# Kernel tuning notes

Hardware: AMD Instinct MI355X
Metric: run time of the kernel (lower is better)

Reference implementation:

```python
import jax, jax.numpy as jnp
import numpy as np

N = 131072      # points (rays x samples chunk)
E = 8           # spatial sub-networks (centroids)
DIN = 90        # encoded pos+dir features fed to sub-NeRFs (xyz_real=True -> x[:, 3:])
H = 256         # sub-NeRF hidden width
DOUT = 4        # rgb + sigma
MARGIN = 2.0    # boundary_margin
EPS = 1e-8


def setup_inputs() -> dict:
    key = jax.random.key(0)
    k = jax.random.split(key, 5)
    x_xyz = jax.random.uniform(k[0], (N, 3), dtype=jnp.float32)          # routing coords in [0,1)^3
    x_feat = jax.random.normal(k[1], (N, DIN), dtype=jnp.float32)        # encoded features
    x = jnp.concatenate([x_xyz, x_feat], axis=1)                         # [N, 3+DIN]
    centroids = jax.random.uniform(k[2], (E, 3), dtype=jnp.float32)
    W1 = jax.random.normal(k[3], (E, DIN, H), dtype=jnp.float32) * 0.05
    b1 = jnp.zeros((E, H), dtype=jnp.float32)
    W2 = jax.random.normal(k[4], (E, H, DOUT), dtype=jnp.float32) * 0.05
    b2 = jnp.zeros((E, DOUT), dtype=jnp.float32)
    return {"x": x, "centroids": centroids, "W1": W1, "b1": b1, "W2": W2, "b2": b2}


def reference(x, centroids, W1, b1, W2, b2):
    # --- centroid routing (torch.cdist equivalent) ---
    xyz = x[:, :3]                                                       # [N,3]
    d2 = jnp.sum((xyz[:, None, :] - centroids[None, :, :]) ** 2, axis=-1)
    dist = jnp.sqrt(jnp.maximum(d2, 0.0))                                # [N,E]
    inv = 1.0 / (dist + EPS)
    min_d = jnp.min(dist, axis=1, keepdims=True)                         # [N,1]
    inv = jnp.where(dist > MARGIN * min_d, 0.0, inv)                     # zero far experts
    weights = inv / jnp.sum(inv, axis=-1, keepdims=True)                 # [N,E], rows sum to 1

    # --- per-expert sub-NeRF MLP, weighted combine ---
    # Dense-equivalent of masked gather + weighted scatter-add: experts whose
    # weight is exactly 0 contribute nothing, matching the torch masked path.
    feat = x[:, 3:]                                                      # xyz_real=True -> drop xyz
    h = jax.nn.relu(jnp.einsum('nd,edh->enh', feat, W1) + b1[:, None, :])  # [E,N,H]
    out_e = jnp.einsum('enh,eho->eno', h, W2) + b2[:, None, :]             # [E,N,DOUT]
    return jnp.einsum('eno,ne->no', out_e, weights)                        # [N,DOUT]
```

## Files before the change

### kernel.cpp

```cpp
#include <hip/hip_runtime.h>

#define NPTS 131072
#define NE 8
#define DIN 90
#define NH 256
#define NGMAX 2304

typedef __attribute__((ext_vector_type(8))) short bf16x8;
typedef __attribute__((ext_vector_type(4))) float f32x4;
typedef __attribute__((ext_vector_type(2))) float f32x2;
typedef __attribute__((ext_vector_type(4))) unsigned int u32x4;
typedef __attribute__((ext_vector_type(2))) unsigned int u32x2;
typedef __attribute__((ext_vector_type(4), aligned(4))) float f32x4a;
typedef __attribute__((ext_vector_type(2), aligned(4))) float f32x2a;

#define WS_W1T   0
#define WS_W2T   393216
#define WS_PERM  458752
#define WS_BKTB  983040
#define WS_HIST  984064
#define WS_CUR   985088
#define WS_GTB   986112
#define WS_GTM   995328
#define WS_END   1004544

__device__ __forceinline__ unsigned short f2bf(float f) {
  unsigned int u = __float_as_uint(f);
  u += 0x7fffu + ((u >> 16) & 1u);
  return (unsigned short)(u >> 16);
}

#if defined(__has_builtin) && __has_builtin(__builtin_amdgcn_cvt_pk_bf16_f32)
typedef __attribute__((ext_vector_type(2))) __bf16 bf16x2;
__device__ __forceinline__ unsigned int pkbf(float f0, float f1) {
  bf16x2 r = __builtin_amdgcn_cvt_pk_bf16_f32(f0, f1);
  return __builtin_bit_cast(unsigned int, r);
}
#else
__device__ __forceinline__ unsigned int pkbf(float f0, float f1) {
  unsigned int u0 = __float_as_uint(f0) + 0x7fffu;
  unsigned int u1 = __float_as_uint(f1) + 0x7fffu;
  return __builtin_amdgcn_perm(u1, u0, 0x07060302u);
}
#endif

__device__ __forceinline__ bf16x8 cvt8(f32x4 a, f32x4 b) {
  u32x4 r;
  r[0] = pkbf(a[0], a[1]);
  r[1] = pkbf(a[2], a[3]);
  r[2] = pkbf(b[0], b[1]);
  r[3] = pkbf(b[2], b[3]);
  return __builtin_bit_cast(bf16x8, r);
}

__device__ __forceinline__ int pmask(const float* __restrict__ gx,
                                     const float* __restrict__ cent) {
  float px = gx[0], py = gx[1], pz = gx[2];
  float d[NE];
  float mind = 3.4e38f;
#pragma unroll
  for (int e = 0; e < NE; ++e) {
    float dx = px - cent[e * 3 + 0];
    float dy = py - cent[e * 3 + 1];
    float dz = pz - cent[e * 3 + 2];
    float d2 = dx * dx + dy * dy + dz * dz;
    d[e] = sqrtf(fmaxf(d2, 0.f));
    mind = fminf(mind, d[e]);
  }
  int m = 0;
#pragma unroll
  for (int e = 0; e < NE; ++e)
    if (!(d[e] > 2.0f * mind)) m |= (1 << e);
  return m;
}

__global__ __launch_bounds__(512) void zerok(int* __restrict__ p) {
  p[threadIdx.x] = 0;
}

__global__ __launch_bounds__(256) void prep_mask(
    const float* __restrict__ W1, const float* __restrict__ W2,
    const float* __restrict__ x, const float* __restrict__ cent,
    unsigned short* __restrict__ W1T, unsigned short* __restrict__ W2T,
    int* __restrict__ hist) {
  const int t = threadIdx.x;
  const int blk = blockIdx.x;
  __shared__ unsigned int shm[64 * 49];
  if (blk < 32) {
    const int e = blk >> 2;
    const int n0 = (blk & 3) * 64;
    const int nl = t & 63;
    const int kq = t >> 6;
#pragma unroll
    for (int j = 0; j < 12; ++j) {
      const int kp2 = kq + 4 * j;
      const int k0 = 2 * kp2, k1 = k0 + 1;
      unsigned int lo = 0, hi = 0;
      if (k0 < DIN) lo = f2bf(W1[((size_t)e * DIN + k0) * NH + n0 + nl]);
      if (k1 < DIN) hi = f2bf(W1[((size_t)e * DIN + k1) * NH + n0 + nl]);
      shm[nl * 49 + kp2] = lo | (hi << 16);
    }
    __syncthreads();
    unsigned int* dst = (unsigned int*)(W1T + (size_t)(e * NH + n0) * 96);
#pragma unroll
    for (int j = 0; j < 12; ++j) {
      const int u = t + 256 * j;
      dst[u] = shm[(u / 48) * 49 + (u % 48)];
    }
  } else if (blk < 40) {
    const int e = blk - 32;
    unsigned int* dst = (unsigned int*)W2T + (size_t)e * 2048;
    const float* src = W2 + (size_t)e * 1024;
#pragma unroll
    for (int j = 0; j < 8; ++j) {
      const int u = t + 256 * j;
      const int o = u >> 7, kp = u & 127;
      unsigned int v = 0;
      if (o < 4) {
        unsigned int lo = f2bf(src[(2 * kp) * 4 + o]);
        unsigned int hi = f2bf(src[(2 * kp + 1) * 4 + o]);
        v = lo | (hi << 16);
      }
      dst[u] = v;
    }
  } else {
    int* lh = (int*)shm;
    lh[t] = 0;
    __syncthreads();
    const int base = (blk - 40) * 1024;
#pragma unroll
    for (int j = 0; j < 4; ++j) {
      const int m = pmask(x + (size_t)(base + j * 256 + t) * 93, cent);
      atomicAdd(&lh[m], 1);
    }
    __syncthreads();
    if (lh[t] > 0) atomicAdd(&hist[t], lh[t]);
  }
}

__global__ __launch_bounds__(256) void scank(const int* __restrict__ hist,
                                             int* __restrict__ bktb,
                                             int* __restrict__ gt_base,
                                             int* __restrict__ gt_meta) {
  __shared__ int s1[256], s2[256];
  const int t = threadIdx.x;
  const int c = hist[t];
  s1[t] = c;
  __syncthreads();
  for (int off = 1; off < 256; off <<= 1) {
    int a = s1[t];
    int b = (t >= off) ? s1[t - off] : 0;
    __syncthreads();
    s1[t] = a + b;
    __syncthreads();
  }
  const int base = s1[t] - c;
  bktb[t] = base;
  const int gc = (c + 63) >> 6;
  s2[t] = gc;
  __syncthreads();
  for (int off = 1; off < 256; off <<= 1) {
    int a = s2[t];
    int b = (t >= off) ? s2[t - off] : 0;
    __syncthreads();
    s2[t] = a + b;
    __syncthreads();
  }
  const int goff = s2[t] - gc;
  for (int j = 0; j < gc; ++j) {
    const int rem = c - 64 * j;
    gt_base[goff + j] = base + 64 * j;
    gt_meta[goff + j] = t | ((rem < 64 ? rem : 64) << 8);
  }
  __syncthreads();
  const int total = s2[255];
  for (int s = total + t; s < NGMAX; s += 256) gt_meta[s] = 0;
}

__global__ __launch_bounds__(256) void scatterk(const float* __restrict__ x,
                                                const float* __restrict__ cent,
                                                const int* __restrict__ bktb,
                                                int* __restrict__ cursor,
                                                int* __restrict__ perm) {
  __shared__ int lh[256], lb[256], lc[256];
  const int t = threadIdx.x;
  lh[t] = 0;
  lc[t] = 0;
  __syncthreads();
  const int base = blockIdx.x * 1024;
  int m[4];
#pragma unroll
  for (int j = 0; j < 4; ++j) {
    m[j] = pmask(x + (size_t)(base + j * 256 + t) * 93, cent);
    atomicAdd(&lh[m[j]], 1);
  }
  __syncthreads();
  if (lh[t] > 0) lb[t] = bktb[t] + atomicAdd(&cursor[t], lh[t]);
  __syncthreads();
#pragma unroll
  for (int j = 0; j < 4; ++j) {
    const int p = base + j * 256 + t;
    const int lp = atomicAdd(&lc[m[j]], 1);
    perm[lb[m[j]] + lp] = p;
  }
}

#define UNRL _Pragma("unroll")

#define LOADW1(E_, C_, D0, D1, D2, D3, D4, D5)                                  \
  do {                                                                          \
    const unsigned short* _p =                                                  \
        W1T + (size_t)((E_) * NH + 128 * (C_) + 32 * wid + l15) * 96 + 8 * l4;  \
    D0 = *(const bf16x8*)(_p);                                                  \
    D1 = *(const bf16x8*)(_p + 32);                                             \
    D2 = *(const bf16x8*)(_p + 64);                                             \
    D3 = *(const bf16x8*)(_p + 1536);                                           \
    D4 = *(const bf16x8*)(_p + 1568);                                           \
    D5 = *(const bf16x8*)(_p + 1600);                                           \
  } while (0)

#define LOADBW(E_, C_, D)                                                       \
  do {                                                                          \
    D = *(const bf16x8*)(W2T + (size_t)((E_) * 16 + l15) * NH + 128 * (C_) +    \
                         32 * wid + 8 * l4);                                    \
  } while (0)

#define EPI(MF)                                                                 \
  UNRL for (int nf = 0; nf < 4; ++nf) {                                         \
    const float _w = wv[nf];                                                    \
    f32x4 _a = acc[nf];                                                         \
    f32x2 _p0, _p1;                                                             \
    _p0[0] = _a[0]; _p0[1] = _a[1];                                             \
    _p1[0] = _a[2]; _p1[1] = _a[3];                                             \
    const f32x2 _z = {0.f, 0.f};                                                \
    _p0 = __builtin_elementwise_max(_p0, _z) * _w;                              \
    _p1 = __builtin_elementwise_max(_p1, _z) * _w;                              \
    u32x2 _pk;                                                                  \
    _pk[0] = pkbf(_p0[0], _p0[1]);                                              \
    _pk[1] = pkbf(_p1[0], _p1[1]);                                              \
    *(u32x2*)&sH[gbase + (nf * 64 + (l15 + 16 * (2 * (MF) + (l4 >> 1)))) * 8 +  \
                 4 * (l4 & 1)] = _pk;                                           \
  }

#define STEP(E_, C_, LDWV_, EP_, CP_, CW0, CW1, CW2, CW3, CW4, CW5, CBW,        \
             NW0, NW1, NW2, NW3, NW4, NW5, NBW)                                 \
  do {                                                                          \
    const int _cb = 128 * (C_) + 32 * wid;                                      \
    f32x4 _b1v0 = *(const f32x4*)&sB1[(E_) * NH + _cb + 4 * l4];                \
    f32x4 _b1v1 = *(const f32x4*)&sB1[(E_) * NH + _cb + 16 + 4 * l4];           \
    if (LDWV_) {                                                                \
      UNRL for (int nf = 0; nf < 4; ++nf) wv[nf] = sW[(E_)][16 * nf + l15];     \
    }                                                                           \
    LOADBW(EP_, CP_, NBW);                                                      \
    LOADW1(EP_, CP_, NW0, NW1, NW2, NW3, NW4, NW5);                             \
    {                                                                           \
      f32x4 acc[4];                                                             \
      __builtin_amdgcn_s_setprio(1);                                            \
      UNRL for (int nf = 0; nf < 4; ++nf)                                       \
          acc[nf] = __builtin_amdgcn_mfma_f32_16x16x32_bf16(CW0, bfr[nf][0],    \
                                                            _b1v0, 0, 0, 0);    \
      UNRL for (int nf = 0; nf < 4; ++nf)                                       \
          acc[nf] = __builtin_amdgcn_mfma_f32_16x16x32_bf16(CW1, bfr[nf][1],    \
                                                            acc[nf], 0, 0, 0);  \
      UNRL for (int nf = 0; nf < 4; ++nf)                                       \
          acc[nf] = __builtin_amdgcn_mfma_f32_16x16x32_bf16(CW2, bfr[nf][2],    \
                                                            acc[nf], 0, 0, 0);  \
      __builtin_amdgcn_s_setprio(0);                                            \
      EPI(0)                                                                    \
      __builtin_amdgcn_s_setprio(1);                                            \
      UNRL for (int nf = 0; nf < 4; ++nf)                                       \
          acc[nf] = __builtin_amdgcn_mfma_f32_16x16x32_bf16(CW3, bfr[nf][0],    \
                                                            _b1v1, 0, 0, 0);    \
      UNRL for (int nf = 0; nf < 4; ++nf)                                       \
          acc[nf] = __builtin_amdgcn_mfma_f32_16x16x32_bf16(CW4, bfr[nf][1],    \
                                                            acc[nf], 0, 0, 0);  \
      UNRL for (int nf = 0; nf < 4; ++nf)                                       \
          acc[nf] = __builtin_amdgcn_mfma_f32_16x16x32_bf16(CW5, bfr[nf][2],    \
                                                            acc[nf], 0, 0, 0);  \
      __builtin_amdgcn_s_setprio(0);                                            \
      EPI(1)                                                                    \
    }                                                                           \
    __builtin_amdgcn_s_setprio(1);                                              \
    UNRL for (int rf = 0; rf < 4; ++rf) {                                       \
      bf16x8 _ah = *(const bf16x8*)&sH[gbase + (rf * 64 + lane) * 8];           \
      facc[rf] = __builtin_amdgcn_mfma_f32_16x16x32_bf16(_ah, CBW, facc[rf],    \
                                                         0, 0, 0);              \
    }                                                                           \
    __builtin_amdgcn_s_setprio(0);                                              \
  } while (0)

__global__ __launch_bounds__(256, 3) void main_sparse(
    const float* __restrict__ x, const float* __restrict__ cent,
    const float* __restrict__ b1, const float* __restrict__ b2,
    const unsigned short* __restrict__ W1T, const unsigned short* __restrict__ W2T,
    const int* __restrict__ perm, const int* __restrict__ gt_base,
    const int* __restrict__ gt_meta, float* __restrict__ out) {
  const int meta = gt_meta[blockIdx.x];
  const int cnt = meta >> 8;
  if (cnt == 0) return;
  const int gmask = meta & 255;
  const int base = gt_base[blockIdx.x];

  __shared__ unsigned short sH[4 * 2048];
  __shared__ float sW[NE][64];
  __shared__ float sB2[64][4];
  __shared__ float sB1[NE * NH];
  __shared__ int sIdx[64];
  __shared__ int sElist[9];

  const int t    = threadIdx.x;
  const int lane = t & 63;
  const int wid  = t >> 6;
  const int l15  = lane & 15;
  const int l4   = lane >> 4;
  const int gbase = wid * 2048;

#pragma unroll
  for (int j = 0; j < 2; ++j)
    *(f32x4*)&sB1[t * 4 + j * 1024] = *(const f32x4a*)&b1[t * 4 + j * 1024];
  if (t < 64) sIdx[t] = perm[base + (t < cnt ? t : cnt - 1)];
  if (t == 0) {
    int ne = 0;
#pragma unroll
    for (int e = 0; e < NE; ++e)
      if ((gmask >> e) & 1) sElist[ne++] = e;
    sElist[8] = ne;
  }
  __syncthreads();

  bf16x8 bfr[4][3];
#pragma unroll
  for (int nf = 0; nf < 4; ++nf) {
    const float* gr = x + (size_t)sIdx[16 * nf + l15] * 93 + 3;
    f32x4 v0, v1;
    v0 = *(const f32x4a*)(gr + 8 * l4);
    v1 = *(const f32x4a*)(gr + 8 * l4 + 4);
    bfr[nf][0] = cvt8(v0, v1);
    v0 = *(const f32x4a*)(gr + 32 + 8 * l4);
    v1 = *(const f32x4a*)(gr + 36 + 8 * l4);
    bfr[nf][1] = cvt8(v0, v1);
    if (l4 < 3) {
      v0 = *(const f32x4a*)(gr + 64 + 8 * l4);
      v1 = *(const f32x4a*)(gr + 68 + 8 * l4);
    } else {
      f32x2 tl = *(const f32x2a*)(gr + 88);
      v0[0] = tl[0]; v0[1] = tl[1]; v0[2] = 0.f; v0[3] = 0.f;
      v1[0] = 0.f; v1[1] = 0.f; v1[2] = 0.f; v1[3] = 0.f;
    }
    bfr[nf][2] = cvt8(v0, v1);
  }

  if (t < 64) {
    const float* gx = x + (size_t)sIdx[t] * 93;
    float px = gx[0], py = gx[1], pz = gx[2];
    float dist[NE], inv[NE];
    float mind = 3.4e38f;
#pragma unroll
    for (int e = 0; e < NE; ++e) {
      float dx = px - cent[e * 3 + 0];
      float dy = py - cent[e * 3 + 1];
      float dz = pz - cent[e * 3 + 2];
      float d2 = dx * dx + dy * dy + dz * dz;
      float d = sqrtf(fmaxf(d2, 0.f));
      dist[e] = d;
      inv[e] = 1.f / (d + 1e-8f);
      mind = fminf(mind, d);
    }
    float s = 0.f;
#pragma unroll
    for (int e = 0; e < NE; ++e) {
      if (dist[e] > 2.0f * mind) inv[e] = 0.f;
      s += inv[e];
    }
    float rs = 1.f / s;
    float bb[4] = {0.f, 0.f, 0.f, 0.f};
#pragma unroll
    for (int e = 0; e < NE; ++e) {
      float w = inv[e] * rs;
      sW[e][t] = w;
#pragma unroll
      for (int o = 0; o < 4; ++o) bb[o] += w * b2[e * 4 + o];
    }
#pragma unroll
    for (int o = 0; o < 4; ++o) sB2[t][o] = bb[o];
  }
  __syncthreads();

  const int niter = 2 * sElist[8];

  bf16x8 w1A0, w1A1, w1A2, w1A3, w1A4, w1A5;
  bf16x8 w1B0, w1B1, w1B2, w1B3, w1B4, w1B5;
  bf16x8 bwA, bwB;
  float wv[4];
  f32x4 facc[4] = {{0.f, 0.f, 0.f, 0.f}, {0.f, 0.f, 0.f, 0.f},
                   {0.f, 0.f, 0.f, 0.f}, {0.f, 0.f, 0.f, 0.f}};

  {
    const int e0 = sElist[0];
    LOADBW(e0, 0, bwA);
    LOADW1(e0, 0, w1A0, w1A1, w1A2, w1A3, w1A4, w1A5);
  }

  for (int i = 0; i < niter; i += 2) {
    const int e = sElist[i >> 1];
    const int ip2 = (i + 2 < niter) ? (i + 2) : (i + 1);
    const int e2 = sElist[ip2 >> 1];
    const int c2 = ip2 & 1;
    STEP(e, 0, 1, e, 1, w1A0, w1A1, w1A2, w1A3, w1A4, w1A5, bwA,
         w1B0, w1B1, w1B2, w1B3, w1B4, w1B5, bwB);
    STEP(e, 1, 0, e2, c2, w1B0, w1B1, w1B2, w1B3, w1B4, w1B5, bwB,
         w1A0, w1A1, w1A2, w1A3, w1A4, w1A5, bwA);
  }

  __syncthreads();
  float* sOutP = (float*)sH;
  if (l15 < 4) {
#pragma unroll
    for (int rf = 0; rf < 4; ++rf)
#pragma unroll
      for (int r = 0; r < 4; ++r)
        sOutP[(wid * 64 + 16 * rf + 4 * l4 + r) * 4 + l15] = facc[rf][r];
  }
  __syncthreads();
  {
    const int row = t >> 2, o = t & 3;
    if (row < cnt) {
      float v = sB2[row][o] + sOutP[(0 * 64 + row) * 4 + o] +
                sOutP[(1 * 64 + row) * 4 + o] + sOutP[(2 * 64 + row) * 4 + o] +
                sOutP[(3 * 64 + row) * 4 + o];
      out[(size_t)sIdx[row] * 4 + o] = v;
    }
  }
}

__global__ __launch_bounds__(256, 3) void meganerf_main(
    const float* __restrict__ x, const float* __restrict__ cent,
    const float* __restrict__ b1, const float* __restrict__ b2,
    const unsigned short* __restrict__ W1T, const unsigned short* __restrict__ W2T,
    float* __restrict__ out) {
  __shared__ unsigned short sH[4 * 2048];
  __shared__ float sW[NE][64];
  __shared__ float sB2[64][4];
  __shared__ float sB1[NE * NH];

  const int t    = threadIdx.x;
  const int lane = t & 63;
  const int wid  = t >> 6;
  const int l15  = lane & 15;
  const int l4   = lane >> 4;
  const int row0 = blockIdx.x * 64;
  const int gbase = wid * 2048;

#pragma unroll
  for (int j = 0; j < 2; ++j)
    *(f32x4*)&sB1[t * 4 + j * 1024] = *(const f32x4a*)&b1[t * 4 + j * 1024];

  bf16x8 bfr[4][3];
#pragma unroll
  for (int nf = 0; nf < 4; ++nf) {
    const float* gr = x + (size_t)(row0 + 16 * nf + l15) * 93 + 3;
    f32x4 v0, v1;
    v0 = *(const f32x4a*)(gr + 8 * l4);
    v1 = *(const f32x4a*)(gr + 8 * l4 + 4);
    bfr[nf][0] = cvt8(v0, v1);
    v0 = *(const f32x4a*)(gr + 32 + 8 * l4);
    v1 = *(const f32x4a*)(gr + 36 + 8 * l4);
    bfr[nf][1] = cvt8(v0, v1);
    if (l4 < 3) {
      v0 = *(const f32x4a*)(gr + 64 + 8 * l4);
      v1 = *(const f32x4a*)(gr + 68 + 8 * l4);
    } else {
      f32x2 tl = *(const f32x2a*)(gr + 88);
      v0[0] = tl[0]; v0[1] = tl[1]; v0[2] = 0.f; v0[3] = 0.f;
      v1[0] = 0.f; v1[1] = 0.f; v1[2] = 0.f; v1[3] = 0.f;
    }
    bfr[nf][2] = cvt8(v0, v1);
  }

  if (t < 64) {
    const float* gx = x + (size_t)(row0 + t) * 93;
    float px = gx[0], py = gx[1], pz = gx[2];
    float dist[NE], inv[NE];
    float mind = 3.4e38f;
#pragma unroll
    for (int e = 0; e < NE; ++e) {
      float dx = px - cent[e * 3 + 0];
      float dy = py - cent[e * 3 + 1];
      float dz = pz - cent[e * 3 + 2];
      float d2 = dx * dx + dy * dy + dz * dz;
      float d = sqrtf(fmaxf(d2, 0.f));
      dist[e] = d;
      inv[e] = 1.f / (d + 1e-8f);
      mind = fminf(mind, d);
    }
    float s = 0.f;
#pragma unroll
    for (int e = 0; e < NE; ++e) {
      if (dist[e] > 2.0f * mind) inv[e] = 0.f;
      s += inv[e];
    }
    float rs = 1.f / s;
    float bb[4] = {0.f, 0.f, 0.f, 0.f};
#pragma unroll
    for (int e = 0; e < NE; ++e) {
      float w = inv[e] * rs;
      sW[e][t] = w;
#pragma unroll
      for (int o = 0; o < 4; ++o) bb[o] += w * b2[e * 4 + o];
    }
#pragma unroll
    for (int o = 0; o < 4; ++o) sB2[t][o] = bb[o];
  }
  __syncthreads();

  bf16x8 w1A0, w1A1, w1A2, w1A3, w1A4, w1A5;
  bf16x8 w1B0, w1B1, w1B2, w1B3, w1B4, w1B5;
  bf16x8 bwA, bwB;
  float wv[4];
  f32x4 facc[4] = {{0.f, 0.f, 0.f, 0.f}, {0.f, 0.f, 0.f, 0.f},
                   {0.f, 0.f, 0.f, 0.f}, {0.f, 0.f, 0.f, 0.f}};

  LOADBW(0, 0, bwA);
  LOADW1(0, 0, w1A0, w1A1, w1A2, w1A3, w1A4, w1A5);

  for (int i = 0; i < 16; i += 2) {
    const int e = i >> 1;
    const int ip2 = (i + 2) & 15;
    const int e2 = ip2 >> 1;
    STEP(e, 0, 1, e, 1, w1A0, w1A1, w1A2, w1A3, w1A4, w1A5, bwA,
         w1B0, w1B1, w1B2, w1B3, w1B4, w1B5, bwB);
    STEP(e, 1, 0, e2, 0, w1B0, w1B1, w1B2, w1B3, w1B4, w1B5, bwB,
         w1A0, w1A1, w1A2, w1A3, w1A4, w1A5, bwA);
  }

  __syncthreads();
  float* sOutP = (float*)sH;
  if (l15 < 4) {
#pragma unroll
    for (int rf = 0; rf < 4; ++rf)
#pragma unroll
      for (int r = 0; r < 4; ++r)
        sOutP[(wid * 64 + 16 * rf + 4 * l4 + r) * 4 + l15] = facc[rf][r];
  }
  __syncthreads();
  {
    const int row = t >> 2, o = t & 3;
    float v = sB2[row][o] + sOutP[(0 * 64 + row) * 4 + o] + sOutP[(1 * 64 + row) * 4 + o] +
              sOutP[(2 * 64 + row) * 4 + o] + sOutP[(3 * 64 + row) * 4 + o];
    out[row0 * 4 + t] = v;
  }
}

extern "C" void kernel_launch(void* const* d_in, const int* in_sizes, int n_in,
                              void* d_out, int out_size, void* d_ws, size_t ws_size,
                              hipStream_t stream) {
  const float* x    = (const float*)d_in[0];
  const float* cent = (const float*)d_in[1];
  const float* W1   = (const float*)d_in[2];
  const float* b1   = (const float*)d_in[3];
  const float* W2   = (const float*)d_in[4];
  const float* b2   = (const float*)d_in[5];
  float* out = (float*)d_out;

  char* ws = (char*)d_ws;
  unsigned short* W1T = (unsigned short*)(ws + WS_W1T);
  unsigned short* W2T = (unsigned short*)(ws + WS_W2T);
  int* perm   = (int*)(ws + WS_PERM);
  int* bktb   = (int*)(ws + WS_BKTB);
  int* hist   = (int*)(ws + WS_HIST);
  int* cursor = (int*)(ws + WS_CUR);
  int* gtb    = (int*)(ws + WS_GTB);
  int* gtm    = (int*)(ws + WS_GTM);

  if (ws_size >= (size_t)WS_END) {
    zerok<<<1, 512, 0, stream>>>(hist);
    prep_mask<<<168, 256, 0, stream>>>(W1, W2, x, cent, W1T, W2T, hist);
    scank<<<1, 256, 0, stream>>>(hist, bktb, gtb, gtm);
    scatterk<<<128, 256, 0, stream>>>(x, cent, bktb, cursor, perm);
    main_sparse<<<NGMAX, 256, 0, stream>>>(x, cent, b1, b2, W1T, W2T, perm, gtb,
                                           gtm, out);
  } else {
    prep_mask<<<40, 256, 0, stream>>>(W1, W2, x, cent, W1T, W2T, hist);
    meganerf_main<<<NPTS / 64, 256, 0, stream>>>(x, cent, b1, b2, W1T, W2T, out);
  }
}
```

Measured before the change: 173.3 us.

## Fuse routing pipeline into one cooperative persistent kernel with grid syncs

```diff
diff --git a/kernel.cpp b/kernel.cpp
--- a/kernel.cpp
+++ b/kernel.cpp
@@ -1,10 +1,13 @@
 #include <hip/hip_runtime.h>
+#include <hip/hip_cooperative_groups.h>
 
 #define NPTS 131072
 #define NE 8
 #define DIN 90
 #define NH 256
 #define NGMAX 2304
+
+namespace cg = cooperative_groups;
 
 typedef __attribute__((ext_vector_type(8))) short bf16x8;
 typedef __attribute__((ext_vector_type(4))) float f32x4;
@@ -17,12 +20,12 @@
 #define WS_W1T   0
 #define WS_W2T   393216
 #define WS_PERM  458752
-#define WS_BKTB  983040
-#define WS_HIST  984064
-#define WS_CUR   985088
-#define WS_GTB   986112
-#define WS_GTM   995328
-#define WS_END   1004544
+#define WS_PHIST 983040
+#define WS_BKTB  1114112
+#define WS_CUR   1115136
+#define WS_GTB   1116160
+#define WS_GTM   1125376
+#define WS_END   1134592
 
 __device__ __forceinline__ unsigned short f2bf(float f) {
   unsigned int u = __float_as_uint(f);
@@ -72,137 +75,6 @@
   for (int e = 0; e < NE; ++e)
     if (!(d[e] > 2.0f * mind)) m |= (1 << e);
   return m;
-}
-
-__global__ __launch_bounds__(512) void zerok(int* __restrict__ p) {
-  p[threadIdx.x] = 0;
-}
-
-__global__ __launch_bounds__(256) void prep_mask(
-    const float* __restrict__ W1, const float* __restrict__ W2,
-    const float* __restrict__ x, const float* __restrict__ cent,
-    unsigned short* __restrict__ W1T, unsigned short* __restrict__ W2T,
-    int* __restrict__ hist) {
-  const int t = threadIdx.x;
-  const int blk = blockIdx.x;
-  __shared__ unsigned int shm[64 * 49];
-  if (blk < 32) {
-    const int e = blk >> 2;
-    const int n0 = (blk & 3) * 64;
-    const int nl = t & 63;
-    const int kq = t >> 6;
-#pragma unroll
-    for (int j = 0; j < 12; ++j) {
-      const int kp2 = kq + 4 * j;
-      const int k0 = 2 * kp2, k1 = k0 + 1;
-      unsigned int lo = 0, hi = 0;
-      if (k0 < DIN) lo = f2bf(W1[((size_t)e * DIN + k0) * NH + n0 + nl]);
-      if (k1 < DIN) hi = f2bf(W1[((size_t)e * DIN + k1) * NH + n0 + nl]);
-      shm[nl * 49 + kp2] = lo | (hi << 16);
-    }
-    __syncthreads();
-    unsigned int* dst = (unsigned int*)(W1T + (size_t)(e * NH + n0) * 96);
-#pragma unroll
-    for (int j = 0; j < 12; ++j) {
-      const int u = t + 256 * j;
-      dst[u] = shm[(u / 48) * 49 + (u % 48)];
-    }
-  } else if (blk < 40) {
-    const int e = blk - 32;
-    unsigned int* dst = (unsigned int*)W2T + (size_t)e * 2048;
-    const float* src = W2 + (size_t)e * 1024;
-#pragma unroll
-    for (int j = 0; j < 8; ++j) {
-      const int u = t + 256 * j;
-      const int o = u >> 7, kp = u & 127;
-      unsigned int v = 0;
-      if (o < 4) {
-        unsigned int lo = f2bf(src[(2 * kp) * 4 + o]);
-        unsigned int hi = f2bf(src[(2 * kp + 1) * 4 + o]);
-        v = lo | (hi << 16);
-      }
-      dst[u] = v;
-    }
-  } else {
-    int* lh = (int*)shm;
-    lh[t] = 0;
-    __syncthreads();
-    const int base = (blk - 40) * 1024;
-#pragma unroll
-    for (int j = 0; j < 4; ++j) {
-      const int m = pmask(x + (size_t)(base + j * 256 + t) * 93, cent);
-      atomicAdd(&lh[m], 1);
-    }
-    __syncthreads();
-    if (lh[t] > 0) atomicAdd(&hist[t], lh[t]);
-  }
-}
-
-__global__ __launch_bounds__(256) void scank(const int* __restrict__ hist,
-                                             int* __restrict__ bktb,
-                                             int* __restrict__ gt_base,
-                                             int* __restrict__ gt_meta) {
-  __shared__ int s1[256], s2[256];
-  const int t = threadIdx.x;
-  const int c = hist[t];
-  s1[t] = c;
-  __syncthreads();
-  for (int off = 1; off < 256; off <<= 1) {
-    int a = s1[t];
-    int b = (t >= off) ? s1[t - off] : 0;
-    __syncthreads();
-    s1[t] = a + b;
-    __syncthreads();
-  }
-  const int base = s1[t] - c;
-  bktb[t] = base;
-  const int gc = (c + 63) >> 6;
-  s2[t] = gc;
-  __syncthreads();
-  for (int off = 1; off < 256; off <<= 1) {
-    int a = s2[t];
-    int b = (t >= off) ? s2[t - off] : 0;
-    __syncthreads();
-    s2[t] = a + b;
-    __syncthreads();
-  }
-  const int goff = s2[t] - gc;
-  for (int j = 0; j < gc; ++j) {
-    const int rem = c - 64 * j;
-    gt_base[goff + j] = base + 64 * j;
-    gt_meta[goff + j] = t | ((rem < 64 ? rem : 64) << 8);
-  }
-  __syncthreads();
-  const int total = s2[255];
-  for (int s = total + t; s < NGMAX; s += 256) gt_meta[s] = 0;
-}
-
-__global__ __launch_bounds__(256) void scatterk(const float* __restrict__ x,
-                                                const float* __restrict__ cent,
-                                                const int* __restrict__ bktb,
-                                                int* __restrict__ cursor,
-                                                int* __restrict__ perm) {
-  __shared__ int lh[256], lb[256], lc[256];
-  const int t = threadIdx.x;
-  lh[t] = 0;
-  lc[t] = 0;
-  __syncthreads();
-  const int base = blockIdx.x * 1024;
-  int m[4];
-#pragma unroll
-  for (int j = 0; j < 4; ++j) {
-    m[j] = pmask(x + (size_t)(base + j * 256 + t) * 93, cent);
-    atomicAdd(&lh[m[j]], 1);
-  }
-  __syncthreads();
-  if (lh[t] > 0) lb[t] = bktb[t] + atomicAdd(&cursor[t], lh[t]);
-  __syncthreads();
-#pragma unroll
-  for (int j = 0; j < 4; ++j) {
-    const int p = base + j * 256 + t;
-    const int lp = atomicAdd(&lc[m[j]], 1);
-    perm[lb[m[j]] + lp] = p;
-  }
 }
 
 #define UNRL _Pragma("unroll")
@@ -289,17 +161,18 @@
     __builtin_amdgcn_s_setprio(0);                                              \
   } while (0)
 
-__global__ __launch_bounds__(256, 3) void main_sparse(
+__global__ __launch_bounds__(256, 3) void mega2(
     const float* __restrict__ x, const float* __restrict__ cent,
     const float* __restrict__ b1, const float* __restrict__ b2,
-    const unsigned short* __restrict__ W1T, const unsigned short* __restrict__ W2T,
-    const int* __restrict__ perm, const int* __restrict__ gt_base,
-    const int* __restrict__ gt_meta, float* __restrict__ out) {
-  const int meta = gt_meta[blockIdx.x];
-  const int cnt = meta >> 8;
-  if (cnt == 0) return;
-  const int gmask = meta & 255;
-  const int base = gt_base[blockIdx.x];
+    const float* __restrict__ W1, const float* __restrict__ W2,
+    float* __restrict__ out,
+    unsigned short* __restrict__ W1T, unsigned short* __restrict__ W2T,
+    int* __restrict__ perm, int* __restrict__ phist, int* __restrict__ bktb,
+    int* __restrict__ cursor, int* __restrict__ gt_base,
+    int* __restrict__ gt_meta) {
+  cg::grid_group gg = cg::this_grid();
+  const int t   = threadIdx.x;
+  const int blk = blockIdx.x;
 
   __shared__ unsigned short sH[4 * 2048];
   __shared__ float sW[NE][64];
@@ -308,7 +181,124 @@
   __shared__ int sIdx[64];
   __shared__ int sElist[9];
 
-  const int t    = threadIdx.x;
+  if (blk < 32) {
+    const int e = blk >> 2;
+    const int n0 = (blk & 3) * 64;
+    unsigned int* ld = (unsigned int*)sH;
+    const int nl = t & 63;
+    const int kq = t >> 6;
+#pragma unroll
+    for (int j = 0; j < 12; ++j) {
+      const int kp2 = kq + 4 * j;
+      const int k0 = 2 * kp2, k1 = k0 + 1;
+      unsigned int lo = 0, hi = 0;
+      if (k0 < DIN) lo = f2bf(W1[((size_t)e * DIN + k0) * NH + n0 + nl]);
+      if (k1 < DIN) hi = f2bf(W1[((size_t)e * DIN + k1) * NH + n0 + nl]);
+      ld[nl * 49 + kp2] = lo | (hi << 16);
+    }
+    __syncthreads();
+    unsigned int* dst = (unsigned int*)(W1T + (size_t)(e * NH + n0) * 96);
+#pragma unroll
+    for (int j = 0; j < 12; ++j) {
+      const int u = t + 256 * j;
+      dst[u] = ld[(u / 48) * 49 + (u % 48)];
+    }
+  } else if (blk < 40) {
+    const int e = blk - 32;
+    unsigned int* dst = (unsigned int*)W2T + (size_t)e * 2048;
+    const float* src = W2 + (size_t)e * 1024;
+#pragma unroll
+    for (int j = 0; j < 8; ++j) {
+      const int u = t + 256 * j;
+      const int o = u >> 7, kp = u & 127;
+      unsigned int v = 0;
+      if (o < 4) {
+        unsigned int lo = f2bf(src[(2 * kp) * 4 + o]);
+        unsigned int hi = f2bf(src[(2 * kp + 1) * 4 + o]);
+        v = lo | (hi << 16);
+      }
+      dst[u] = v;
+    }
+  } else if (blk < 168) {
+    int* lh = (int*)sH;
+    lh[t] = 0;
+    __syncthreads();
+    const int base = (blk - 40) * 1024;
+#pragma unroll
+    for (int j = 0; j < 4; ++j) {
+      const int m = pmask(x + (size_t)(base + j * 256 + t) * 93, cent);
+      atomicAdd(&lh[m], 1);
+    }
+    __syncthreads();
+    phist[(blk - 40) * 256 + t] = lh[t];
+  }
+  gg.sync();
+
+  if (blk == 0) {
+    int* s1 = (int*)sH;
+    int* s2 = (int*)sH + 256;
+    int c = 0;
+    for (int b = 0; b < 128; ++b) c += phist[b * 256 + t];
+    s1[t] = c;
+    __syncthreads();
+    for (int off = 1; off < 256; off <<= 1) {
+      int a = s1[t];
+      int bb = (t >= off) ? s1[t - off] : 0;
+      __syncthreads();
+      s1[t] = a + bb;
+      __syncthreads();
+    }
+    const int base = s1[t] - c;
+    bktb[t] = base;
+    const int gc = (c + 63) >> 6;
+    s2[t] = gc;
+    __syncthreads();
+    for (int off = 1; off < 256; off <<= 1) {
+      int a = s2[t];
+      int bb = (t >= off) ? s2[t - off] : 0;
+      __syncthreads();
+      s2[t] = a + bb;
+      __syncthreads();
+    }
+    const int goff = s2[t] - gc;
+    for (int j = 0; j < gc; ++j) {
+      const int rem = c - 64 * j;
+      gt_base[goff + j] = base + 64 * j;
+      gt_meta[goff + j] = t | ((rem < 64 ? rem : 64) << 8);
+    }
+    cursor[t] = 0;
+    __syncthreads();
+    const int total = s2[255];
+    for (int s = total + t; s < NGMAX; s += 256) gt_meta[s] = 0;
+  }
+  gg.sync();
+
+  if (blk < 128) {
+    int* lh = (int*)sH;
+    int* lb = (int*)sH + 256;
+    int* lc = (int*)sH + 512;
+    lh[t] = 0;
+    lc[t] = 0;
+    __syncthreads();
+    const int base = blk * 1024;
+    int m[4];
+#pragma unroll
+    for (int j = 0; j < 4; ++j) {
+      m[j] = pmask(x + (size_t)(base + j * 256 + t) * 93, cent);
+      atomicAdd(&lh[m[j]], 1);
+    }
+    __syncthreads();
+    if (lh[t] > 0) lb[t] = bktb[t] + atomicAdd(&cursor[t], lh[t]);
+    __syncthreads();
+#pragma unroll
+    for (int j = 0; j < 4; ++j) {
+      const int p = base + j * 256 + t;
+      const int lp = atomicAdd(&lc[m[j]], 1);
+      perm[lb[m[j]] + lp] = p;
+    }
+  }
+  gg.sync();
+
   const int lane = t & 63;
   const int wid  = t >> 6;
   const int l15  = lane & 15;
@@ -318,117 +308,174 @@
 #pragma unroll
   for (int j = 0; j < 2; ++j)
     *(f32x4*)&sB1[t * 4 + j * 1024] = *(const f32x4a*)&b1[t * 4 + j * 1024];
-  if (t < 64) sIdx[t] = perm[base + (t < cnt ? t : cnt - 1)];
-  if (t == 0) {
-    int ne = 0;
-#pragma unroll
-    for (int e = 0; e < NE; ++e)
-      if ((gmask >> e) & 1) sElist[ne++] = e;
-    sElist[8] = ne;
-  }
-  __syncthreads();
-
-  bf16x8 bfr[4][3];
-#pragma unroll
-  for (int nf = 0; nf < 4; ++nf) {
-    const float* gr = x + (size_t)sIdx[16 * nf + l15] * 93 + 3;
-    f32x4 v0, v1;
-    v0 = *(const f32x4a*)(gr + 8 * l4);
-    v1 = *(const f32x4a*)(gr + 8 * l4 + 4);
-    bfr[nf][0] = cvt8(v0, v1);
-    v0 = *(const f32x4a*)(gr + 32 + 8 * l4);
-    v1 = *(const f32x4a*)(gr + 36 + 8 * l4);
-    bfr[nf][1] = cvt8(v0, v1);
-    if (l4 < 3) {
-      v0 = *(const f32x4a*)(gr + 64 + 8 * l4);
-      v1 = *(const f32x4a*)(gr + 68 + 8 * l4);
-    } else {
-      f32x2 tl = *(const f32x2a*)(gr + 88);
-      v0[0] = tl[0]; v0[1] = tl[1]; v0[2] = 0.f; v0[3] = 0.f;
-      v1[0] = 0.f; v1[1] = 0.f; v1[2] = 0.f; v1[3] = 0.f;
-    }
-    bfr[nf][2] = cvt8(v0, v1);
-  }
-
-  if (t < 64) {
-    const float* gx = x + (size_t)sIdx[t] * 93;
-    float px = gx[0], py = gx[1], pz = gx[2];
-    float dist[NE], inv[NE];
-    float mind = 3.4e38f;
-#pragma unroll
-    for (int e = 0; e < NE; ++e) {
-      float dx = px - cent[e * 3 + 0];
-      float dy = py - cent[e * 3 + 1];
-      float dz = pz - cent[e * 3 + 2];
-      float d2 = dx * dx + dy * dy + dz * dz;
-      float d = sqrtf(fmaxf(d2, 0.f));
-      dist[e] = d;
-      inv[e] = 1.f / (d + 1e-8f);
-      mind = fminf(mind, d);
-    }
-    float s = 0.f;
-#pragma unroll
-    for (int e = 0; e < NE; ++e) {
-      if (dist[e] > 2.0f * mind) inv[e] = 0.f;
-      s += inv[e];
-    }
-    float rs = 1.f / s;
-    float bb[4] = {0.f, 0.f, 0.f, 0.f};
-#pragma unroll
-    for (int e = 0; e < NE; ++e) {
-      float w = inv[e] * rs;
-      sW[e][t] = w;
-#pragma unroll
-      for (int o = 0; o < 4; ++o) bb[o] += w * b2[e * 4 + o];
-    }
-#pragma unroll
-    for (int o = 0; o < 4; ++o) sB2[t][o] = bb[o];
-  }
-  __syncthreads();
-
-  const int niter = 2 * sElist[8];
-
-  bf16x8 w1A0, w1A1, w1A2, w1A3, w1A4, w1A5;
-  bf16x8 w1B0, w1B1, w1B2, w1B3, w1B4, w1B5;
-  bf16x8 bwA, bwB;
-  float wv[4];
-  f32x4 facc[4] = {{0.f, 0.f, 0.f, 0.f}, {0.f, 0.f, 0.f, 0.f},
-                   {0.f, 0.f, 0.f, 0.f}, {0.f, 0.f, 0.f, 0.f}};
-
-  {
-    const int e0 = sElist[0];
-    LOADBW(e0, 0, bwA);
-    LOADW1(e0, 0, w1A0, w1A1, w1A2, w1A3, w1A4, w1A5);
-  }
-
-  for (int i = 0; i < niter; i += 2) {
-    const int e = sElist[i >> 1];
-    const int ip2 = (i + 2 < niter) ? (i + 2) : (i + 1);
-    const int e2 = sElist[ip2 >> 1];
-    const int c2 = ip2 & 1;
-    STEP(e, 0, 1, e, 1, w1A0, w1A1, w1A2, w1A3, w1A4, w1A5, bwA,
-         w1B0, w1B1, w1B2, w1B3, w1B4, w1B5, bwB);
-    STEP(e, 1, 0, e2, c2, w1B0, w1B1, w1B2, w1B3, w1B4, w1B5, bwB,
-         w1A0, w1A1, w1A2, w1A3, w1A4, w1A5, bwA);
-  }
-
-  __syncthreads();
-  float* sOutP = (float*)sH;
-  if (l15 < 4) {
-#pragma unroll
-    for (int rf = 0; rf < 4; ++rf)
-#pragma unroll
-      for (int r = 0; r < 4; ++r)
-        sOutP[(wid * 64 + 16 * rf + 4 * l4 + r) * 4 + l15] = facc[rf][r];
-  }
-  __syncthreads();
-  {
-    const int row = t >> 2, o = t & 3;
-    if (row < cnt) {
-      float v = sB2[row][o] + sOutP[(0 * 64 + row) * 4 + o] +
-                sOutP[(1 * 64 + row) * 4 + o] + sOutP[(2 * 64 + row) * 4 + o] +
-                sOutP[(3 * 64 + row) * 4 + o];
-      out[(size_t)sIdx[row] * 4 + o] = v;
+
+  for (int g = blk; g < NGMAX; g += gridDim.x) {
+    const int meta = gt_meta[g];
+    const int cnt = meta >> 8;
+    if (cnt == 0) continue;
+    const int gmask = meta & 255;
+    const int base = gt_base[g];
+
+    __syncthreads();
+    if (t < 64) sIdx[t] = perm[base + (t < cnt ? t : cnt - 1)];
+    if (t == 0) {
+      int ne = 0;
+#pragma unroll
+      for (int e = 0; e < NE; ++e)
+        if ((gmask >> e) & 1) sElist[ne++] = e;
+      sElist[8] = ne;
+    }
+    __syncthreads();
+
+    bf16x8 bfr[4][3];
+#pragma unroll
+    for (int nf = 0; nf < 4; ++nf) {
+      const float* gr = x + (size_t)sIdx[16 * nf + l15] * 93 + 3;
+      f32x4 v0, v1;
+      v0 = *(const f32x4a*)(gr + 8 * l4);
+      v1 = *(const f32x4a*)(gr + 8 * l4 + 4);
+      bfr[nf][0] = cvt8(v0, v1);
+      v0 = *(const f32x4a*)(gr + 32 + 8 * l4);
+      v1 = *(const f32x4a*)(gr + 36 + 8 * l4);
+      bfr[nf][1] = cvt8(v0, v1);
+      if (l4 < 3) {
+        v0 = *(const f32x4a*)(gr + 64 + 8 * l4);
+        v1 = *(const f32x4a*)(gr + 68 + 8 * l4);
+      } else {
+        f32x2 tl = *(const f32x2a*)(gr + 88);
+        v0[0] = tl[0]; v0[1] = tl[1]; v0[2] = 0.f; v0[3] = 0.f;
+        v1[0] = 0.f; v1[1] = 0.f; v1[2] = 0.f; v1[3] = 0.f;
+      }
+      bfr[nf][2] = cvt8(v0, v1);
+    }
+
+    if (t < 64) {
+      const float* gx = x + (size_t)sIdx[t] * 93;
+      float px = gx[0], py = gx[1], pz = gx[2];
+      float dist[NE], inv[NE];
+      float mind = 3.4e38f;
+#pragma unroll
+      for (int e = 0; e < NE; ++e) {
+        float dx = px - cent[e * 3 + 0];
+        float dy = py - cent[e * 3 + 1];
+        float dz = pz - cent[e * 3 + 2];
+        float d2 = dx * dx + dy * dy + dz * dz;
+        float d = sqrtf(fmaxf(d2, 0.f));
+        dist[e] = d;
+        inv[e] = 1.f / (d + 1e-8f);
+        mind = fminf(mind, d);
+      }
+      float s = 0.f;
+#pragma unroll
+      for (int e = 0; e < NE; ++e) {
+        if (dist[e] > 2.0f * mind) inv[e] = 0.f;
+        s += inv[e];
+      }
+      float rs = 1.f / s;
+      float bb[4] = {0.f, 0.f, 0.f, 0.f};
+#pragma unroll
+      for (int e = 0; e < NE; ++e) {
+        float w = inv[e] * rs;
+        sW[e][t] = w;
+#pragma unroll
+        for (int o = 0; o < 4; ++o) bb[o] += w * b2[e * 4 + o];
+      }
+#pragma unroll
+      for (int o = 0; o < 4; ++o) sB2[t][o] = bb[o];
+    }
+    __syncthreads();
+
+    const int niter = 2 * sElist[8];
+
+    bf16x8 w1A0, w1A1, w1A2, w1A3, w1A4, w1A5;
+    bf16x8 w1B0, w1B1, w1B2, w1B3, w1B4, w1B5;
+    bf16x8 bwA, bwB;
+    float wv[4];
+    f32x4 facc[4] = {{0.f, 0.f, 0.f, 0.f}, {0.f, 0.f, 0.f, 0.f},
+                     {0.f, 0.f, 0.f, 0.f}, {0.f, 0.f, 0.f, 0.f}};
+
+    {
+      const int e0 = sElist[0];
+      LOADBW(e0, 0, bwA);
+      LOADW1(e0, 0, w1A0, w1A1, w1A2, w1A3, w1A4, w1A5);
+    }
+
+    for (int i = 0; i < niter; i += 2) {
+      const int e = sElist[i >> 1];
+      const int ip2 = (i + 2 < niter) ? (i + 2) : (i + 1);
+      const int e2 = sElist[ip2 >> 1];
+      const int c2 = ip2 & 1;
+      STEP(e, 0, 1, e, 1, w1A0, w1A1, w1A2, w1A3, w1A4, w1A5, bwA,
+           w1B0, w1B1, w1B2, w1B3, w1B4, w1B5, bwB);
+      STEP(e, 1, 0, e2, c2, w1B0, w1B1, w1B2, w1B3, w1B4, w1B5, bwB,
+           w1A0, w1A1, w1A2, w1A3, w1A4, w1A5, bwA);
+    }
+
+    __syncthreads();
+    float* sOutP = (float*)sH;
+    if (l15 < 4) {
+#pragma unroll
+      for (int rf = 0; rf < 4; ++rf)
+#pragma unroll
+        for (int r = 0; r < 4; ++r)
+          sOutP[(wid * 64 + 16 * rf + 4 * l4 + r) * 4 + l15] = facc[rf][r];
+    }
+    __syncthreads();
+    {
+      const int row = t >> 2, o = t & 3;
+      if (row < cnt) {
+        float v = sB2[row][o] + sOutP[(0 * 64 + row) * 4 + o] +
+                  sOutP[(1 * 64 + row) * 4 + o] + sOutP[(2 * 64 + row) * 4 + o] +
+                  sOutP[(3 * 64 + row) * 4 + o];
+        out[(size_t)sIdx[row] * 4 + o] = v;
+      }
+    }
+  }
+}
+
+__global__ __launch_bounds__(256) void prep(const float* __restrict__ W1,
+                                            const float* __restrict__ W2,
+                                            unsigned short* __restrict__ W1T,
+                                            unsigned short* __restrict__ W2T) {
+  const int t = threadIdx.x;
+  if (blockIdx.x < 32) {
+    const int e = blockIdx.x >> 2;
+    const int n0 = (blockIdx.x & 3) * 64;
+    __shared__ unsigned int ld[64][49];
+    const int nl = t & 63;
+    const int kq = t >> 6;
+#pragma unroll
+    for (int j = 0; j < 12; ++j) {
+      const int kp2 = kq + 4 * j;
+      const int k0 = 2 * kp2, k1 = k0 + 1;
+      unsigned int lo = 0, hi = 0;
+      if (k0 < DIN) lo = f2bf(W1[((size_t)e * DIN + k0) * NH + n0 + nl]);
+      if (k1 < DIN) hi = f2bf(W1[((size_t)e * DIN + k1) * NH + n0 + nl]);
+      ld[nl][kp2] = lo | (hi << 16);
+    }
+    __syncthreads();
+    unsigned int* dst = (unsigned int*)(W1T + (size_t)(e * NH + n0) * 96);
+#pragma unroll
+    for (int j = 0; j < 12; ++j) {
+      const int u = t + 256 * j;
+      dst[u] = ld[u / 48][u % 48];
+    }
+  } else {
+    const int e = blockIdx.x - 32;
+    unsigned int* dst = (unsigned int*)W2T + (size_t)e * 2048;
+    const float* src = W2 + (size_t)e * 1024;
+#pragma unroll
+    for (int j = 0; j < 8; ++j) {
+      const int u = t + 256 * j;
+      const int o = u >> 7;
+      const int kp = u & 127;
+      unsigned int v = 0;
+      if (o < 4) {
+        unsigned int lo = f2bf(src[(2 * kp) * 4 + o]);
+        unsigned int hi = f2bf(src[(2 * kp + 1) * 4 + o]);
+        v = lo | (hi << 16);
+      }
+      dst[u] = v;
     }
   }
 }
@@ -566,21 +613,37 @@
   unsigned short* W1T = (unsigned short*)(ws + WS_W1T);
   unsigned short* W2T = (unsigned short*)(ws + WS_W2T);
   int* perm   = (int*)(ws + WS_PERM);
+  int* phist  = (int*)(ws + WS_PHIST);
   int* bktb   = (int*)(ws + WS_BKTB);
-  int* hist   = (int*)(ws + WS_HIST);
   int* cursor = (int*)(ws + WS_CUR);
   int* gtb    = (int*)(ws + WS_GTB);
   int* gtm    = (int*)(ws + WS_GTM);
 
-  if (ws_size >= (size_t)WS_END) {
-    zerok<<<1, 512, 0, stream>>>(hist);
-    prep_mask<<<168, 256, 0, stream>>>(W1, W2, x, cent, W1T, W2T, hist);
-    scank<<<1, 256, 0, stream>>>(hist, bktb, gtb, gtm);
-    scatterk<<<128, 256, 0, stream>>>(x, cent, bktb, cursor, perm);
-    main_sparse<<<NGMAX, 256, 0, stream>>>(x, cent, b1, b2, W1T, W2T, perm, gtb,
-                                           gtm, out);
-  } else {
-    prep_mask<<<40, 256, 0, stream>>>(W1, W2, x, cent, W1T, W2T, hist);
+  static int nblk = -2;
+  if (nblk == -2) {
+    int bpc = 0;
+    if (hipOccupancyMaxActiveBlocksPerMultiprocessor(&bpc, mega2, 256, 0) ==
+            hipSuccess && bpc > 0) {
+      long nb = (long)bpc * 256;
+      nblk = nb > NGMAX ? NGMAX : (int)nb;
+    } else {
+      nblk = -1;
+    }
+  }
+
+  bool ok = false;
+  if (nblk >= 168 && ws_size >= (size_t)WS_END) {
+    const float *xa = x, *ca = cent, *b1a = b1, *b2a = b2, *W1a = W1, *W2a = W2;
+    float* oa = out;
+    unsigned short *w1t = W1T, *w2t = W2T;
+    int *pm = perm, *ph = phist, *bb = bktb, *cu = cursor, *g1 = gtb, *g2 = gtm;
+    void* args[] = {&xa, &ca, &b1a, &b2a, &W1a, &W2a, &oa,
+                    &w1t, &w2t, &pm, &ph, &bb, &cu, &g1, &g2};
+    ok = hipLaunchCooperativeKernel(mega2, dim3(nblk), dim3(256), args, 0,
+                                    stream) == hipSuccess;
+  }
+  if (!ok) {
+    prep<<<40, 256, 0, stream>>>(W1, W2, W1T, W2T);
     meganerf_main<<<NPTS / 64, 256, 0, stream>>>(x, cent, b1, b2, W1T, W2T, out);
   }
 }
```

New measurement: 307.4 us. 77.4% more time.

## Merge histogram scan and scatter into one kernel using per-block histograms

Applied to the files above, without the earlier changes.

```diff
diff --git a/kernel.cpp b/kernel.cpp
--- a/kernel.cpp
+++ b/kernel.cpp
@@ -17,12 +17,10 @@
 #define WS_W1T   0
 #define WS_W2T   393216
 #define WS_PERM  458752
-#define WS_BKTB  983040
-#define WS_HIST  984064
-#define WS_CUR   985088
-#define WS_GTB   986112
-#define WS_GTM   995328
-#define WS_END   1004544
+#define WS_PHIST 983040
+#define WS_GTB   1114112
+#define WS_GTM   1123328
+#define WS_END   1132544
 
 __device__ __forceinline__ unsigned short f2bf(float f) {
   unsigned int u = __float_as_uint(f);
@@ -74,21 +72,29 @@
   return m;
 }
 
-__global__ __launch_bounds__(512) void zerok(int* __restrict__ p) {
-  p[threadIdx.x] = 0;
-}
-
-__global__ __launch_bounds__(256) void prep_mask(
+__global__ __launch_bounds__(256) void prep_mask2(
     const float* __restrict__ W1, const float* __restrict__ W2,
     const float* __restrict__ x, const float* __restrict__ cent,
     unsigned short* __restrict__ W1T, unsigned short* __restrict__ W2T,
-    int* __restrict__ hist) {
+    int* __restrict__ phist) {
   const int t = threadIdx.x;
   const int blk = blockIdx.x;
   __shared__ unsigned int shm[64 * 49];
-  if (blk < 32) {
-    const int e = blk >> 2;
-    const int n0 = (blk & 3) * 64;
+  if (blk < 128) {
+    int* lh = (int*)shm;
+    lh[t] = 0;
+    __syncthreads();
+    const int base = blk * 1024;
+#pragma unroll
+    for (int j = 0; j < 4; ++j) {
+      const int m = pmask(x + (size_t)(base + j * 256 + t) * 93, cent);
+      atomicAdd(&lh[m], 1);
+    }
+    __syncthreads();
+    phist[blk * 256 + t] = lh[t];
+  } else if (blk < 160) {
+    const int e = (blk - 128) >> 2;
+    const int n0 = ((blk - 128) & 3) * 64;
     const int nl = t & 63;
     const int kq = t >> 6;
 #pragma unroll
@@ -107,8 +113,8 @@
       const int u = t + 256 * j;
       dst[u] = shm[(u / 48) * 49 + (u % 48)];
     }
-  } else if (blk < 40) {
-    const int e = blk - 32;
+  } else {
+    const int e = blk - 160;
     unsigned int* dst = (unsigned int*)W2T + (size_t)e * 2048;
     const float* src = W2 + (size_t)e * 1024;
 #pragma unroll
@@ -123,85 +129,66 @@
       }
       dst[u] = v;
     }
-  } else {
-    int* lh = (int*)shm;
-    lh[t] = 0;
-    __syncthreads();
-    const int base = (blk - 40) * 1024;
-#pragma unroll
-    for (int j = 0; j < 4; ++j) {
-      const int m = pmask(x + (size_t)(base + j * 256 + t) * 93, cent);
-      atomicAdd(&lh[m], 1);
-    }
-    __syncthreads();
-    if (lh[t] > 0) atomicAdd(&hist[t], lh[t]);
-  }
-}
-
-__global__ __launch_bounds__(256) void scank(const int* __restrict__ hist,
-                                             int* __restrict__ bktb,
-                                             int* __restrict__ gt_base,
-                                             int* __restrict__ gt_meta) {
-  __shared__ int s1[256], s2[256];
+  }
+}
+
+__global__ __launch_bounds__(256) void scatter_tables(
+    const float* __restrict__ x, const float* __restrict__ cent,
+    const int* __restrict__ phist, int* __restrict__ perm,
+    int* __restrict__ gt_base, int* __restrict__ gt_meta) {
+  __shared__ int s1[256], s2[256], lbs[256], lc[256];
   const int t = threadIdx.x;
-  const int c = hist[t];
+  const int b = blockIdx.x;
+
+  int c = 0, pre = 0;
+  for (int bb = 0; bb < 128; ++bb) {
+    const int v = phist[bb * 256 + t];
+    pre += (bb < b) ? v : 0;
+    c += v;
+  }
   s1[t] = c;
   __syncthreads();
   for (int off = 1; off < 256; off <<= 1) {
     int a = s1[t];
-    int b = (t >= off) ? s1[t - off] : 0;
-    __syncthreads();
-    s1[t] = a + b;
-    __syncthreads();
-  }
-  const int base = s1[t] - c;
-  bktb[t] = base;
-  const int gc = (c + 63) >> 6;
-  s2[t] = gc;
-  __syncthreads();
-  for (int off = 1; off < 256; off <<= 1) {
-    int a = s2[t];
-    int b = (t >= off) ? s2[t - off] : 0;
-    __syncthreads();
-    s2[t] = a + b;
-    __syncthreads();
-  }
-  const int goff = s2[t] - gc;
-  for (int j = 0; j < gc; ++j) {
-    const int rem = c - 64 * j;
-    gt_base[goff + j] = base + 64 * j;
-    gt_meta[goff + j] = t | ((rem < 64 ? rem : 64) << 8);
-  }
-  __syncthreads();
-  const int total = s2[255];
-  for (int s = total + t; s < NGMAX; s += 256) gt_meta[s] = 0;
-}
-
-__global__ __launch_bounds__(256) void scatterk(const float* __restrict__ x,
-                                                const float* __restrict__ cent,
-                                                const int* __restrict__ bktb,
-                                                int* __restrict__ cursor,
-                                                int* __restrict__ perm) {
-  __shared__ int lh[256], lb[256], lc[256];
-  const int t = threadIdx.x;
-  lh[t] = 0;
+    int v = (t >= off) ? s1[t - off] : 0;
+    __syncthreads();
+    s1[t] = a + v;
+    __syncthreads();
+  }
+  const int bkbase = s1[t] - c;
+  lbs[t] = bkbase + pre;
   lc[t] = 0;
-  __syncthreads();
-  const int base = blockIdx.x * 1024;
-  int m[4];
+
+  if (b == 0) {
+    const int gc = (c + 63) >> 6;
+    s2[t] = gc;
+    __syncthreads();
+    for (int off = 1; off < 256; off <<= 1) {
+      int a = s2[t];
+      int v = (t >= off) ? s2[t - off] : 0;
+      __syncthreads();
+      s2[t] = a + v;
+      __syncthreads();
+    }
+    const int goff = s2[t] - gc;
+    for (int j = 0; j < gc; ++j) {
+      const int rem = c - 64 * j;
+      gt_base[goff + j] = bkbase + 64 * j;
+      gt_meta[goff + j] = t | ((rem < 64 ? rem : 64) << 8);
+    }
+    __syncthreads();
+    const int total = s2[255];
+    for (int s = total + t; s < NGMAX; s += 256) gt_meta[s] = 0;
+  }
+  __syncthreads();
+
+  const int pbase = b * 1024;
 #pragma unroll
   for (int j = 0; j < 4; ++j) {
-    m[j] = pmask(x + (size_t)(base + j * 256 + t) * 93, cent);
-    atomicAdd(&lh[m[j]], 1);
-  }
-  __syncthreads();
-  if (lh[t] > 0) lb[t] = bktb[t] + atomicAdd(&cursor[t], lh[t]);
-  __syncthreads();
-#pragma unroll
-  for (int j = 0; j < 4; ++j) {
-    const int p = base + j * 256 + t;
-    const int lp = atomicAdd(&lc[m[j]], 1);
-    perm[lb[m[j]] + lp] = p;
+    const int p = pbase + j * 256 + t;
+    const int m = pmask(x + (size_t)p * 93, cent);
+    const int lp = atomicAdd(&lc[m], 1);
+    perm[lbs[m] + lp] = p;
   }
 }
 
@@ -305,7 +292,6 @@
   __shared__ float sW[NE][64];
   __shared__ float sB2[64][4];
   __shared__ float sB1[NE * NH];
-  __shared__ int sIdx[64];
   __shared__ int sElist[9];
 
   const int t    = threadIdx.x;
@@ -318,20 +304,13 @@
 #pragma unroll
   for (int j = 0; j < 2; ++j)
     *(f32x4*)&sB1[t * 4 + j * 1024] = *(const f32x4a*)&b1[t * 4 + j * 1024];
-  if (t < 64) sIdx[t] = perm[base + (t < cnt ? t : cnt - 1)];
-  if (t == 0) {
-    int ne = 0;
-#pragma unroll
-    for (int e = 0; e < NE; ++e)
-      if ((gmask >> e) & 1) sElist[ne++] = e;
-    sElist[8] = ne;
-  }
-  __syncthreads();
 
   bf16x8 bfr[4][3];
 #pragma unroll
   for (int nf = 0; nf < 4; ++nf) {
-    const float* gr = x + (size_t)sIdx[16 * nf + l15] * 93 + 3;
+    const int r = 16 * nf + l15;
+    const int pidx = perm[base + (r < cnt ? r : cnt - 1)];
+    const float* gr = x + (size_t)pidx * 93 + 3;
     f32x4 v0, v1;
     v0 = *(const f32x4a*)(gr + 8 * l4);
     v1 = *(const f32x4a*)(gr + 8 * l4 + 4);
@@ -350,8 +329,10 @@
     bfr[nf][2] = cvt8(v0, v1);
   }
 
-  if (t < 64) {
-    const float* gx = x + (size_t)sIdx[t] * 93;
+  if (lane < 16) {
+    const int pt = 16 * wid + lane;
+    const int pidx = perm[base + (pt < cnt ? pt : cnt - 1)];
+    const float* gx = x + (size_t)pidx * 93;
     float px = gx[0], py = gx[1], pz = gx[2];
     float dist[NE], inv[NE];
     float mind = 3.4e38f;
@@ -377,12 +358,19 @@
 #pragma unroll
     for (int e = 0; e < NE; ++e) {
       float w = inv[e] * rs;
-      sW[e][t] = w;
+      sW[e][pt] = w;
 #pragma unroll
       for (int o = 0; o < 4; ++o) bb[o] += w * b2[e * 4 + o];
     }
 #pragma unroll
-    for (int o = 0; o < 4; ++o) sB2[t][o] = bb[o];
+    for (int o = 0; o < 4; ++o) sB2[pt][o] = bb[o];
+  }
+  if (t == 0) {
+    int ne = 0;
+#pragma unroll
+    for (int e = 0; e < NE; ++e)
+      if ((gmask >> e) & 1) sElist[ne++] = e;
+    sElist[8] = ne;
   }
   __syncthreads();
 
@@ -425,10 +413,58 @@
   {
     const int row = t >> 2, o = t & 3;
     if (row < cnt) {
+      const int pidx = perm[base + row];
       float v = sB2[row][o] + sOutP[(0 * 64 + row) * 4 + o] +
                 sOutP[(1 * 64 + row) * 4 + o] + sOutP[(2 * 64 + row) * 4 + o] +
                 sOutP[(3 * 64 + row) * 4 + o];
-      out[(size_t)sIdx[row] * 4 + o] = v;
+      out[(size_t)pidx * 4 + o] = v;
+    }
+  }
+}
+
+__global__ __launch_bounds__(256) void prep(const float* __restrict__ W1,
+                                            const float* __restrict__ W2,
+                                            unsigned short* __restrict__ W1T,
+                                            unsigned short* __restrict__ W2T) {
+  const int t = threadIdx.x;
+  if (blockIdx.x < 32) {
+    const int e = blockIdx.x >> 2;
+    const int n0 = (blockIdx.x & 3) * 64;
+    __shared__ unsigned int ld[64][49];
+    const int nl = t & 63;
+    const int kq = t >> 6;
+#pragma unroll
+    for (int j = 0; j < 12; ++j) {
+      const int kp2 = kq + 4 * j;
+      const int k0 = 2 * kp2, k1 = k0 + 1;
+      unsigned int lo = 0, hi = 0;
+      if (k0 < DIN) lo = f2bf(W1[((size_t)e * DIN + k0) * NH + n0 + nl]);
+      if (k1 < DIN) hi = f2bf(W1[((size_t)e * DIN + k1) * NH + n0 + nl]);
+      ld[nl][kp2] = lo | (hi << 16);
+    }
+    __syncthreads();
+    unsigned int* dst = (unsigned int*)(W1T + (size_t)(e * NH + n0) * 96);
+#pragma unroll
+    for (int j = 0; j < 12; ++j) {
+      const int u = t + 256 * j;
+      dst[u] = ld[u / 48][u % 48];
+    }
+  } else {
+    const int e = blockIdx.x - 32;
+    unsigned int* dst = (unsigned int*)W2T + (size_t)e * 2048;
+    const float* src = W2 + (size_t)e * 1024;
+#pragma unroll
+    for (int j = 0; j < 8; ++j) {
+      const int u = t + 256 * j;
+      const int o = u >> 7;
+      const int kp = u & 127;
+      unsigned int v = 0;
+      if (o < 4) {
+        unsigned int lo = f2bf(src[(2 * kp) * 4 + o]);
+        unsigned int hi = f2bf(src[(2 * kp + 1) * 4 + o]);
+        v = lo | (hi << 16);
+      }
+      dst[u] = v;
     }
   }
 }
@@ -565,22 +601,18 @@
   char* ws = (char*)d_ws;
   unsigned short* W1T = (unsigned short*)(ws + WS_W1T);
   unsigned short* W2T = (unsigned short*)(ws + WS_W2T);
-  int* perm   = (int*)(ws + WS_PERM);
-  int* bktb   = (int*)(ws + WS_BKTB);
-  int* hist   = (int*)(ws + WS_HIST);
-  int* cursor = (int*)(ws + WS_CUR);
-  int* gtb    = (int*)(ws + WS_GTB);
-  int* gtm    = (int*)(ws + WS_GTM);
+  int* perm  = (int*)(ws + WS_PERM);
+  int* phist = (int*)(ws + WS_PHIST);
+  int* gtb   = (int*)(ws + WS_GTB);
+  int* gtm   = (int*)(ws + WS_GTM);
 
   if (ws_size >= (size_t)WS_END) {
-    zerok<<<1, 512, 0, stream>>>(hist);
-    prep_mask<<<168, 256, 0, stream>>>(W1, W2, x, cent, W1T, W2T, hist);
-    scank<<<1, 256, 0, stream>>>(hist, bktb, gtb, gtm);
-    scatterk<<<128, 256, 0, stream>>>(x, cent, bktb, cursor, perm);
+    prep_mask2<<<168, 256, 0, stream>>>(W1, W2, x, cent, W1T, W2T, phist);
+    scatter_tables<<<128, 256, 0, stream>>>(x, cent, phist, perm, gtb, gtm);
     main_sparse<<<NGMAX, 256, 0, stream>>>(x, cent, b1, b2, W1T, W2T, perm, gtb,
                                            gtm, out);
   } else {
-    prep_mask<<<40, 256, 0, stream>>>(W1, W2, x, cent, W1T, W2T, hist);
+    prep<<<40, 256, 0, stream>>>(W1, W2, W1T, W2T);
     meganerf_main<<<NPTS / 64, 256, 0, stream>>>(x, cent, b1, b2, W1T, W2T, out);
   }
 }
```

Result: no change. 171.9 us (-0.8%).
